# Performance work log

Measured on AMD Instinct MI355X. Metric: run time of the kernel, lower is better.

Reference implementation:

```python
import jax, jax.numpy as jnp
import numpy as np

# config matching init_kwargs: stox_params=[4,2,1,1,64,2], in=64, out=128, k=3, pad=1
A_BITS = 4          # a_slices = a_bits / a_bits_per_stream = 4
W_SLICES = 2        # w_bits / w_bits_per_slice = 2
NUM_CHUNKS = 9      # ceil(64*9/64)
SUB = 64            # crossbar chunk width
ITERS = 2           # stochastic iterations
EPS = 1e-5          # BatchNorm1d eps


def ste(y, x):
    # straight-through estimator: forward y, backward identity of x
    return x + jax.lax.stop_gradient(y - x)


def unfold3x3(x):
    # torch F.unfold(x, 3, dilation=1, padding=1, stride=1): [B,C,H,W] -> [B, C*9, H*W]
    B, C, H, W = x.shape
    xp = jnp.pad(x, ((0, 0), (0, 0), (1, 1), (1, 1)))
    cols = [xp[:, :, i:i + H, j:j + W] for i in range(3) for j in range(3)]
    return jnp.stack(cols, axis=2).reshape(B, C * 9, H * W)  # (c, kh, kw) ordering


def setup_inputs() -> dict:
    key = jax.random.key(0)
    k1, k2 = jax.random.split(key)
    inputs = jax.random.normal(k1, (8, 64, 32, 32), jnp.float32)
    fan_in = 64 * 9  # kaiming_normal_ fan_in
    weight = jax.random.normal(k2, (128 * W_SLICES, 64, 3, 3), jnp.float32) * np.float32(np.sqrt(2.0 / fan_in))
    bn_gamma = jnp.ones((128 * W_SLICES,), jnp.float32)
    bn_beta = jnp.zeros((128 * W_SLICES,), jnp.float32)
    return {"inputs": inputs, "weight": weight, "bn_gamma": bn_gamma, "bn_beta": bn_beta}


def reference(inputs, weight, bn_gamma, bn_beta):
    O = weight.shape[0]  # out_channels * W_SLICES = 256
    # --- per-output-row weight standardization + 1-bit STE quantization (WeightQuantize) ---
    wf = weight.reshape(O, -1)                       # [O, Cin*9]
    bw = wf - wf.mean(-1, keepdims=True)
    bw = bw / bw.std(-1, ddof=1, keepdims=True)      # torch std is unbiased
    qw = ste(jnp.sign(bw), bw)                       # [O, Cin*9]
    # --- unfold + multi-bit input stream (create_input_stream): bit-planes stacked on batch dim ---
    a = unfold3x3(inputs)                            # [B, Cin*9, L]
    Bsz, C9, L = a.shape
    x = jnp.clip(a, 0.0, 1.0)
    q = jnp.round(x * (2 ** A_BITS - 1))
    bits = jnp.stack([jnp.floor(q / (2 ** i)) % 2 for i in range(A_BITS)], 0)  # [A,B,C9,L]
    qa = bits.reshape(A_BITS * Bsz, C9, L)
    # --- chunked crossbar linear + BatchNorm1d(train) + MTJ sign, summed over chunks/iterations ---
    out = jnp.zeros((A_BITS * Bsz, O, L), a.dtype)
    for c in range(NUM_CHUNKS):
        wk = qa[:, c * SUB:(c + 1) * SUB, :]         # [B', SUB, L]
        ww = qw[:, c * SUB:(c + 1) * SUB]            # [O, SUB]
        for _ in range(ITERS):
            lin = jnp.einsum('bcl,oc->bol', wk, ww)  # [B', O, L]
            mu = lin.mean((0, 2), keepdims=True)
            var = lin.var((0, 2), keepdims=True)     # biased, as torch BN training
            bn = bn_gamma[None, :, None] * (lin - mu) / jnp.sqrt(var + EPS) + bn_beta[None, :, None]
            out = out + ste(jnp.sign(bn), bn)        # MTJ stochastic comparator -> sign w/ STE
    # --- bit-weighted reconstructions ---
    wvec = (2.0 ** jnp.arange(W_SLICES, dtype=a.dtype)) / (2 ** W_SLICES - 1)
    out = jnp.einsum('s,bsol->bol', wvec, out.reshape(A_BITS * Bsz, W_SLICES, O // W_SLICES, L))
    avec = (2.0 ** jnp.arange(A_BITS, dtype=a.dtype)) / (2 ** A_BITS - 1)
    out = jnp.einsum('a,abol->bol', avec, out.reshape(A_BITS, Bsz, O // W_SLICES, L))
    # --- F.fold with (1,1) kernel == reshape to square spatial map ---
    P = int(np.sqrt(L))
    return out.reshape(Bsz, O // W_SLICES, P, P)
```

## Files before the change

### kernel.cpp

```cpp
#include <hip/hip_runtime.h>
#include <cstdint>
#include <cstddef>

static const size_t OFF_ACT  = 0;
static const size_t OFF_W    = OFF_ACT + 2359296;
static const size_t OFF_T    = OFF_W   + 18432;
static const size_t OFF_S1   = OFF_T   + 18432;
static const size_t OFF_MUG  = OFF_S1  + 9216;
static const size_t OFF_FLAG = OFF_MUG + 18432;

__device__ __forceinline__ int isgn(int e) {
  int t = e < -1 ? -1 : e;
  return t > 1 ? 1 : t;
}

__global__ __launch_bounds__(256) void k_prep(const float* __restrict__ x,
                                              const float* __restrict__ w,
                                              const float* __restrict__ gamma,
                                              const float* __restrict__ beta,
                                              int* __restrict__ T,
                                              uint64_t* __restrict__ act,
                                              uint64_t* __restrict__ wbits,
                                              int* __restrict__ flag) {
  int bid = blockIdx.x;
  int tid = threadIdx.x;
  if (bid < 512) {
    int base = bid << 10;
    int vals[9];
#pragma unroll
    for (int k = 0; k < 9; ++k) vals[k] = 0;
#pragma unroll
    for (int i = 0; i < 4; ++i) {
      int px = tid + i * 256;
      int h = px >> 5, ww = px & 31;
      float v = x[base + px];
      v = fminf(fmaxf(v, 0.f), 1.f);
      int q = (int)rintf(v * 15.f);
      int pc = __popc((unsigned)q);
      vals[0] += pc;
      if (h == 0) vals[1] += pc;
      if (h == 31) vals[2] += pc;
      if (ww == 0) vals[3] += pc;
      if (ww == 31) vals[4] += pc;
      if (h == 0 && ww == 0) vals[5] += pc;
      if (h == 0 && ww == 31) vals[6] += pc;
      if (h == 31 && ww == 0) vals[7] += pc;
      if (h == 31 && ww == 31) vals[8] += pc;
    }
#pragma unroll
    for (int k = 0; k < 9; ++k)
      for (int off = 32; off; off >>= 1) vals[k] += __shfl_down(vals[k], off, 64);
    __shared__ int red[4][9];
    int wid = tid >> 6, lane = tid & 63;
    if (lane == 0)
#pragma unroll
      for (int k = 0; k < 9; ++k) red[wid][k] = vals[k];
    __syncthreads();
    if (tid < 9) T[bid * 9 + tid] = red[0][tid] + red[1][tid] + red[2][tid] + red[3][tid];
  } else if (bid < 1664) {
    int gidx = (bid - 512) * 256 + tid;
    int half = gidx & 3;
    int idx = gidx >> 2;
    int l = idx & 1023;
    int c = (idx >> 10) % 9;
    int b = idx / (9 * 1024);
    int h = l >> 5, w0 = l & 31;
    int i9 = c * 64 + half * 16;
    int ch = i9 / 9;
    int k = i9 - ch * 9;
    int ki = k / 3, kj = k - ki * 3;
    unsigned m0 = 0, m1 = 0, m2 = 0, m3 = 0;
#pragma unroll
    for (int jj = 0; jj < 16; ++jj) {
      int hh = h + ki - 1, ww = w0 + kj - 1;
      int q = 0;
      if ((unsigned)hh < 32u && (unsigned)ww < 32u) {
        float v = x[(((b * 64 + ch) << 10) + (hh << 5)) + ww];
        v = fminf(fmaxf(v, 0.f), 1.f);
        q = (int)rintf(v * 15.f);
      }
      m0 |= (unsigned)(q & 1) << jj;
      m1 |= (unsigned)((q >> 1) & 1) << jj;
      m2 |= (unsigned)((q >> 2) & 1) << jj;
      m3 |= (unsigned)((q >> 3) & 1) << jj;
      if (++kj == 3) { kj = 0; if (++ki == 3) { ki = 0; ++ch; } }
    }
    size_t stride = 8 * 9 * 1024;
    size_t off = ((size_t)b * 9 + c) * 1024 + l;
    unsigned short* a16 = (unsigned short*)act;
    a16[(0 * stride + off) * 4 + half] = (unsigned short)m0;
    a16[(1 * stride + off) * 4 + half] = (unsigned short)m1;
    a16[(2 * stride + off) * 4 + half] = (unsigned short)m2;
    a16[(3 * stride + off) * 4 + half] = (unsigned short)m3;
  } else {
    int lane = tid & 63;
    int wid = tid >> 6;
    int o = (bid - 1664) * 4 + wid;
    const float* row = w + (size_t)o * 576;
    double s = 0.0;
#pragma unroll
    for (int i = 0; i < 9; ++i) s += (double)row[lane + i * 64];
    for (int off = 32; off; off >>= 1) s += __shfl_down(s, off, 64);
    s = __shfl(s, 0, 64);
    float mean = (float)(s / 576.0);
#pragma unroll
    for (int c = 0; c < 9; ++c) {
      float v = row[c * 64 + lane];
      unsigned long long m = __ballot((v - mean) > 0.f);
      if (lane == 0) wbits[o * 9 + c] = (uint64_t)m;
    }
    if (lane == 0) flag[o] = (beta[o] == 0.f && gamma[o] > 0.f) ? 1 : 0;
  }
}

__global__ __launch_bounds__(256) void k_s1(const int* __restrict__ T,
                                            const uint64_t* __restrict__ wbits,
                                            const int* __restrict__ flag,
                                            const float* __restrict__ gamma,
                                            const uint64_t* __restrict__ act,
                                            int* __restrict__ S1,
                                            float2* __restrict__ MUG) {
  __shared__ int Tsh[576];
  __shared__ int Ush[9 * 65];
  int tid = threadIdx.x;
  for (int i = tid; i < 576; i += 256) {
    int acc = 0;
#pragma unroll
    for (int b = 0; b < 8; ++b) acc += T[b * 576 + i];
    Tsh[i] = acc;
  }
  __syncthreads();
  for (int i = tid; i < 576; i += 256) {
    int ch = i / 9;
    int k = i - ch * 9;
    int ki = k / 3, kj = k - ki * 3;
    const int* t = &Tsh[ch * 9];
    int u = t[0];
    if (ki == 0) u -= t[2]; else if (ki == 2) u -= t[1];
    if (kj == 0) u -= t[4]; else if (kj == 2) u -= t[3];
    if (ki == 0 && kj == 0) u += t[8];
    if (ki == 0 && kj == 2) u += t[7];
    if (ki == 2 && kj == 0) u += t[6];
    if (ki == 2 && kj == 2) u += t[5];
    Ush[(i >> 6) * 65 + (i & 63)] = u;
  }
  __syncthreads();
  int pair = blockIdx.x * 256 + tid;
  int o = pair / 9, c = pair - o * 9;
  uint64_t wv = wbits[pair];
  int tot = 0, pos = 0;
#pragma unroll 8
  for (int j = 0; j < 64; ++j) {
    int cnt = Ush[c * 65 + j];
    tot += cnt;
    if ((wv >> j) & 1) pos += cnt;
  }
  int s1 = 2 * pos - tot;
  S1[pair] = s1;
  if (!flag[o]) {
    int s2 = 0;
    for (int i = 0; i < 32768; ++i) {
      uint64_t av = act[((size_t)(i >> 10) * 9 + c) * 1024 + (i & 1023)];
      int lin = 2 * __popcll(av & wv) - __popcll(av);
      s2 += lin * lin;
    }
    float mu = (float)s1 * (1.f / 32768.f);
    float ex2 = (float)s2 * (1.f / 32768.f);
    float var = ex2 - mu * mu;
    if (var < 0.f) var = 0.f;
    MUG[pair] = make_float2(mu, gamma[o] / sqrtf(var + 1e-5f));
  }
}

__global__ __launch_bounds__(256, 8) void k_out(const uint64_t* __restrict__ act,
                                                const uint64_t* __restrict__ wbits,
                                                const int* __restrict__ S1,
                                                const float2* __restrict__ MUG,
                                                const int* __restrict__ flag,
                                                const float* __restrict__ beta,
                                                float* __restrict__ out) {
  int ltile = blockIdx.x;
  int og = blockIdx.y;
  int b = blockIdx.z;
  int tid = threadIdx.x;
  int lane = tid & 63;
  int wid = __builtin_amdgcn_readfirstlane(tid >> 6);
  int op = og * 4 + wid;
  int l = (ltile << 7) + lane * 2;

  uint64_t Wv[2][9];
  int Sv[2][9];
  int FL[2];
#pragma unroll
  for (int s = 0; s < 2; ++s) {
    int o = s * 128 + op;
    FL[s] = flag[o];
#pragma unroll
    for (int c = 0; c < 9; ++c) {
      Wv[s][c] = wbits[o * 9 + c];
      Sv[s][c] = S1[o * 9 + c];
    }
  }

  int M0 = 0, M1 = 0;

  if (FL[0] & FL[1]) {
    for (int a = 0; a < 4; ++a) {
      const uint64_t* ap = act + ((size_t)(a * 8 + b) * 9) * 1024 + l;
      int m00 = 0, m01 = 0, m10 = 0, m11 = 0;
#pragma unroll
      for (int c = 0; c < 9; ++c) {
        uint64_t av0 = ap[c * 1024];
        uint64_t av1 = ap[c * 1024 + 1];
        int np0 = -((int)__popcll(av0) << 15);
        int np1 = -((int)__popcll(av1) << 15);
        {
          uint64_t w = Wv[0][c];
          int t1 = Sv[0][c];
          m00 += isgn((((int)__popcll(av0 & w)) << 16) + np0 - t1);
          m01 += isgn((((int)__popcll(av1 & w)) << 16) + np1 - t1);
        }
        {
          uint64_t w = Wv[1][c];
          int t1 = Sv[1][c];
          m10 += isgn((((int)__popcll(av0 & w)) << 16) + np0 - t1);
          m11 += isgn((((int)__popcll(av1 & w)) << 16) + np1 - t1);
        }
      }
      M0 += (m00 + 2 * m10) << a;
      M1 += (m01 + 2 * m11) << a;
    }
    size_t ob = ((size_t)b * 128 + op) * 1024 + l;
    out[ob]     = (float)M0 * (2.f / 45.f);
    out[ob + 1] = (float)M1 * (2.f / 45.f);
  } else {
    const float avec[4] = {1.f / 15.f, 2.f / 15.f, 4.f / 15.f, 8.f / 15.f};
    const float wvec[2] = {1.f / 3.f, 2.f / 3.f};
    float accf0 = 0.f, accf1 = 0.f;
    for (int a = 0; a < 4; ++a) {
      const uint64_t* ap = act + ((size_t)(a * 8 + b) * 9) * 1024 + l;
      int m00 = 0, m01 = 0, m10 = 0, m11 = 0;
      float f00 = 0.f, f01 = 0.f, f10 = 0.f, f11 = 0.f;
      for (int c = 0; c < 9; ++c) {
        uint64_t av0 = ap[c * 1024];
        uint64_t av1 = ap[c * 1024 + 1];
        int np0 = -((int)__popcll(av0) << 15);
        int np1 = -((int)__popcll(av1) << 15);
        for (int s = 0; s < 2; ++s) {
          uint64_t w = Wv[s][c];
          if (FL[s]) {
            int t1 = Sv[s][c];
            int e0 = (((int)__popcll(av0 & w)) << 16) + np0 - t1;
            int e1 = (((int)__popcll(av1 & w)) << 16) + np1 - t1;
            int g0 = isgn(e0), g1 = isgn(e1);
            if (s == 0) { m00 += g0; m01 += g1; } else { m10 += g0; m11 += g1; }
          } else {
            int o = s * 128 + op;
            float2 m2 = MUG[o * 9 + c];
            float bb = beta[o];
            int l0 = 2 * (int)__popcll(av0 & w) + (np0 >> 15);
            int l1 = 2 * (int)__popcll(av1 & w) + (np1 >> 15);
            float bn0 = m2.y * ((float)l0 - m2.x) + bb;
            float bn1 = m2.y * ((float)l1 - m2.x) + bb;
            float g0 = (bn0 > 0.f) ? 1.f : ((bn0 < 0.f) ? -1.f : 0.f);
            float g1 = (bn1 > 0.f) ? 1.f : ((bn1 < 0.f) ? -1.f : 0.f);
            if (s == 0) { f00 += g0; f01 += g1; } else { f10 += g0; f11 += g1; }
          }
        }
      }
      M0 += (m00 + 2 * m10) << a;
      M1 += (m01 + 2 * m11) << a;
      accf0 += avec[a] * (wvec[0] * f00 + wvec[1] * f10);
      accf1 += avec[a] * (wvec[0] * f01 + wvec[1] * f11);
    }
    size_t ob = ((size_t)b * 128 + op) * 1024 + l;
    out[ob]     = (float)M0 * (2.f / 45.f) + 2.f * accf0;
    out[ob + 1] = (float)M1 * (2.f / 45.f) + 2.f * accf1;
  }
}

extern "C" void kernel_launch(void* const* d_in, const int* in_sizes, int n_in,
                              void* d_out, int out_size, void* d_ws, size_t ws_size,
                              hipStream_t stream) {
  const float* inputs = (const float*)d_in[0];
  const float* weight = (const float*)d_in[1];
  const float* gamma = (const float*)d_in[2];
  const float* beta = (const float*)d_in[3];
  float* out = (float*)d_out;

  char* ws = (char*)d_ws;
  uint64_t* act = (uint64_t*)(ws + OFF_ACT);
  uint64_t* wbits = (uint64_t*)(ws + OFF_W);
  int* T = (int*)(ws + OFF_T);
  int* S1 = (int*)(ws + OFF_S1);
  float2* MUG = (float2*)(ws + OFF_MUG);
  int* flag = (int*)(ws + OFF_FLAG);

  k_prep<<<1728, 256, 0, stream>>>(inputs, weight, gamma, beta, T, act, wbits, flag);
  k_s1<<<9, 256, 0, stream>>>(T, wbits, flag, gamma, act, S1, MUG);
  k_out<<<dim3(8, 32, 8), 256, 0, stream>>>(act, wbits, S1, MUG, flag, beta, out);
}
```

Before: 102.7 us.

## Fuse S1/BN-stat kernel into output kernel, computing per-block stats in shared memory

Removes the separate 9-block k_s1 launch and recomputes the T reduction, U correction and S1 sums redundantly inside every k_out block, restricted to the 8 output rows that block needs. The results live in shared memory, and S1 and flag are broadcast with readfirstlane. This removes one launch and a serialized low-occupancy kernel. In exchange, each of the 2048 blocks redoes the T reduction and S1 work. In the non-flag path each block would also rerun the 32768-iteration variance loop, which would be very costly, but with the default gamma=1 and beta=0 inputs that path is skipped.

```diff
diff --git a/kernel.cpp b/kernel.cpp
--- a/kernel.cpp
+++ b/kernel.cpp
@@ -113,20 +113,24 @@
   }
 }
 
-__global__ __launch_bounds__(256) void k_s1(const int* __restrict__ T,
-                                            const uint64_t* __restrict__ wbits,
-                                            const int* __restrict__ flag,
-                                            const float* __restrict__ gamma,
-                                            const uint64_t* __restrict__ act,
-                                            int* __restrict__ S1,
-                                            float2* __restrict__ MUG) {
+__global__ __launch_bounds__(256, 8) void k_out(const uint64_t* __restrict__ act,
+                                                const uint64_t* __restrict__ wbits,
+                                                const int* __restrict__ T,
+                                                const int* __restrict__ flag,
+                                                const float* __restrict__ gamma,
+                                                const float* __restrict__ beta,
+                                                float* __restrict__ out) {
   __shared__ int Tsh[576];
   __shared__ int Ush[9 * 65];
+  __shared__ int S1sh[72];
+  __shared__ float2 MUGsh[72];
   int tid = threadIdx.x;
+  int og = blockIdx.y;
+
   for (int i = tid; i < 576; i += 256) {
     int acc = 0;
 #pragma unroll
-    for (int b = 0; b < 8; ++b) acc += T[b * 576 + i];
+    for (int bb = 0; bb < 8; ++bb) acc += T[bb * 576 + i];
     Tsh[i] = acc;
   }
   __syncthreads();
@@ -145,44 +149,38 @@
     Ush[(i >> 6) * 65 + (i & 63)] = u;
   }
   __syncthreads();
-  int pair = blockIdx.x * 256 + tid;
-  int o = pair / 9, c = pair - o * 9;
-  uint64_t wv = wbits[pair];
-  int tot = 0, pos = 0;
+  if (tid < 72) {
+    int oi = tid / 9, c = tid - oi * 9;
+    int s = oi >> 2, w = oi & 3;
+    int o = s * 128 + og * 4 + w;
+    uint64_t wv = wbits[o * 9 + c];
+    int tot = 0, pos = 0;
 #pragma unroll 8
-  for (int j = 0; j < 64; ++j) {
-    int cnt = Ush[c * 65 + j];
-    tot += cnt;
-    if ((wv >> j) & 1) pos += cnt;
-  }
-  int s1 = 2 * pos - tot;
-  S1[pair] = s1;
-  if (!flag[o]) {
-    int s2 = 0;
-    for (int i = 0; i < 32768; ++i) {
-      uint64_t av = act[((size_t)(i >> 10) * 9 + c) * 1024 + (i & 1023)];
-      int lin = 2 * __popcll(av & wv) - __popcll(av);
-      s2 += lin * lin;
-    }
-    float mu = (float)s1 * (1.f / 32768.f);
-    float ex2 = (float)s2 * (1.f / 32768.f);
-    float var = ex2 - mu * mu;
-    if (var < 0.f) var = 0.f;
-    MUG[pair] = make_float2(mu, gamma[o] / sqrtf(var + 1e-5f));
-  }
-}
-
-__global__ __launch_bounds__(256, 8) void k_out(const uint64_t* __restrict__ act,
-                                                const uint64_t* __restrict__ wbits,
-                                                const int* __restrict__ S1,
-                                                const float2* __restrict__ MUG,
-                                                const int* __restrict__ flag,
-                                                const float* __restrict__ beta,
-                                                float* __restrict__ out) {
+    for (int j = 0; j < 64; ++j) {
+      int cnt = Ush[c * 65 + j];
+      tot += cnt;
+      if ((wv >> j) & 1) pos += cnt;
+    }
+    int s1 = 2 * pos - tot;
+    S1sh[tid] = s1;
+    if (!flag[o]) {
+      int s2 = 0;
+      for (int i = 0; i < 32768; ++i) {
+        uint64_t av = act[((size_t)(i >> 10) * 9 + c) * 1024 + (i & 1023)];
+        int lin = 2 * __popcll(av & wv) - __popcll(av);
+        s2 += lin * lin;
+      }
+      float mu = (float)s1 * (1.f / 32768.f);
+      float ex2 = (float)s2 * (1.f / 32768.f);
+      float var = ex2 - mu * mu;
+      if (var < 0.f) var = 0.f;
+      MUGsh[tid] = make_float2(mu, gamma[o] / sqrtf(var + 1e-5f));
+    }
+  }
+  __syncthreads();
+
   int ltile = blockIdx.x;
-  int og = blockIdx.y;
   int b = blockIdx.z;
-  int tid = threadIdx.x;
   int lane = tid & 63;
   int wid = __builtin_amdgcn_readfirstlane(tid >> 6);
   int op = og * 4 + wid;
@@ -194,11 +192,11 @@
 #pragma unroll
   for (int s = 0; s < 2; ++s) {
     int o = s * 128 + op;
-    FL[s] = flag[o];
+    FL[s] = __builtin_amdgcn_readfirstlane(flag[o]);
 #pragma unroll
     for (int c = 0; c < 9; ++c) {
       Wv[s][c] = wbits[o * 9 + c];
-      Sv[s][c] = S1[o * 9 + c];
+      Sv[s][c] = __builtin_amdgcn_readfirstlane(S1sh[(s * 4 + wid) * 9 + c]);
     }
   }
 
@@ -255,9 +253,8 @@
             int g0 = isgn(e0), g1 = isgn(e1);
             if (s == 0) { m00 += g0; m01 += g1; } else { m10 += g0; m11 += g1; }
           } else {
-            int o = s * 128 + op;
-            float2 m2 = MUG[o * 9 + c];
-            float bb = beta[o];
+            float2 m2 = MUGsh[(s * 4 + wid) * 9 + c];
+            float bb = beta[s * 128 + op];
             int l0 = 2 * (int)__popcll(av0 & w) + (np0 >> 15);
             int l1 = 2 * (int)__popcll(av1 & w) + (np1 >> 15);
             float bn0 = m2.y * ((float)l0 - m2.x) + bb;
@@ -292,11 +289,8 @@
   uint64_t* act = (uint64_t*)(ws + OFF_ACT);
   uint64_t* wbits = (uint64_t*)(ws + OFF_W);
   int* T = (int*)(ws + OFF_T);
-  int* S1 = (int*)(ws + OFF_S1);
-  float2* MUG = (float2*)(ws + OFF_MUG);
   int* flag = (int*)(ws + OFF_FLAG);
 
   k_prep<<<1728, 256, 0, stream>>>(inputs, weight, gamma, beta, T, act, wbits, flag);
-  k_s1<<<9, 256, 0, stream>>>(T, wbits, flag, gamma, act, S1, MUG);
-  k_out<<<dim3(8, 32, 8), 256, 0, stream>>>(act, wbits, S1, MUG, flag, beta, out);
-}
+  k_out<<<dim3(8, 32, 8), 256, 0, stream>>>(act, wbits, T, flag, gamma, beta, out);
+}
```

Result: no change. 103.1 us (+0.4%).

## Compute binary crossbar dot products with int8 MFMA instead of popcount

Applied to the files above, without the earlier changes.

Weights are now also written as ±1 int8 bytes. In the output kernel, 16 activation bits at a time are expanded into 0/1 bytes, and the 64-wide chunk dot products are computed with 16x16x64 int8 MFMA instructions rather than per-thread popcounts. Work is regrouped so that each block covers 16 spatial positions and all 128 output pairs, and the negated S1 thresholds are staged in shared memory. This adds bit-to-byte unpacking overhead and lowers the occupancy hint in exchange for matrix-core throughput.

```diff
diff --git a/kernel.cpp b/kernel.cpp
--- a/kernel.cpp
+++ b/kernel.cpp
@@ -5,9 +5,12 @@
 static const size_t OFF_ACT  = 0;
 static const size_t OFF_W    = OFF_ACT + 2359296;
 static const size_t OFF_T    = OFF_W   + 18432;
-static const size_t OFF_S1   = OFF_T   + 18432;
-static const size_t OFF_MUG  = OFF_S1  + 9216;
+static const size_t OFF_NS1  = OFF_T   + 18432;
+static const size_t OFF_MUG  = OFF_NS1 + 9216;
 static const size_t OFF_FLAG = OFF_MUG + 18432;
+static const size_t OFF_WB   = OFF_FLAG + 1024;
+
+typedef int v4i __attribute__((ext_vector_type(4)));
 
 __device__ __forceinline__ int isgn(int e) {
   int t = e < -1 ? -1 : e;
@@ -21,7 +24,8 @@
                                               int* __restrict__ T,
                                               uint64_t* __restrict__ act,
                                               uint64_t* __restrict__ wbits,
-                                              int* __restrict__ flag) {
+                                              int* __restrict__ flag,
+                                              signed char* __restrict__ wbyte) {
   int bid = blockIdx.x;
   int tid = threadIdx.x;
   if (bid < 512) {
@@ -106,8 +110,10 @@
 #pragma unroll
     for (int c = 0; c < 9; ++c) {
       float v = row[c * 64 + lane];
-      unsigned long long m = __ballot((v - mean) > 0.f);
+      int pos = (v - mean) > 0.f;
+      unsigned long long m = __ballot(pos);
       if (lane == 0) wbits[o * 9 + c] = (uint64_t)m;
+      wbyte[(c * 256 + o) * 64 + lane] = pos ? (signed char)1 : (signed char)-1;
     }
     if (lane == 0) flag[o] = (beta[o] == 0.f && gamma[o] > 0.f) ? 1 : 0;
   }
@@ -118,7 +124,7 @@
                                             const int* __restrict__ flag,
                                             const float* __restrict__ gamma,
                                             const uint64_t* __restrict__ act,
-                                            int* __restrict__ S1,
+                                            int* __restrict__ negS1,
                                             float2* __restrict__ MUG) {
   __shared__ int Tsh[576];
   __shared__ int Ush[9 * 65];
@@ -156,7 +162,7 @@
     if ((wv >> j) & 1) pos += cnt;
   }
   int s1 = 2 * pos - tot;
-  S1[pair] = s1;
+  negS1[c * 256 + o] = -s1;
   if (!flag[o]) {
     int s2 = 0;
     for (int i = 0; i < 32768; ++i) {
@@ -172,110 +178,128 @@
   }
 }
 
-__global__ __launch_bounds__(256, 8) void k_out(const uint64_t* __restrict__ act,
-                                                const uint64_t* __restrict__ wbits,
-                                                const int* __restrict__ S1,
+__global__ __launch_bounds__(256, 2) void k_out(const uint64_t* __restrict__ act,
+                                                const signed char* __restrict__ wbyte,
+                                                const int* __restrict__ negS1g,
                                                 const float2* __restrict__ MUG,
                                                 const int* __restrict__ flag,
                                                 const float* __restrict__ beta,
                                                 float* __restrict__ out) {
-  int ltile = blockIdx.x;
-  int og = blockIdx.y;
-  int b = blockIdx.z;
+  __shared__ int nsh[2304];
   int tid = threadIdx.x;
+  int lt = blockIdx.x;
+  int b = blockIdx.y;
+  for (int i = tid; i < 2304; i += 256) nsh[i] = negS1g[i];
+  __syncthreads();
+
   int lane = tid & 63;
-  int wid = __builtin_amdgcn_readfirstlane(tid >> 6);
-  int op = og * 4 + wid;
-  int l = (ltile << 7) + lane * 2;
-
-  uint64_t Wv[2][9];
-  int Sv[2][9];
-  int FL[2];
-#pragma unroll
-  for (int s = 0; s < 2; ++s) {
-    int o = s * 128 + op;
-    FL[s] = flag[o];
-#pragma unroll
+  int w = __builtin_amdgcn_readfirstlane(tid >> 6);
+  int row = lane & 15;
+  int g = lane >> 4;
+
+  int o0 = w * 32 + (lane & 31);
+  int fb = flag[o0] & flag[o0 + 128];
+  bool fastAll = (bool)__all(fb != 0);
+
+  const v4i zacc = {0, 0, 0, 0};
+  int l = lt * 16 + row;
+
+  if (fastAll) {
+    int M[2][4] = {{0, 0, 0, 0}, {0, 0, 0, 0}};
     for (int c = 0; c < 9; ++c) {
-      Wv[s][c] = wbits[o * 9 + c];
-      Sv[s][c] = S1[o * 9 + c];
-    }
-  }
-
-  int M0 = 0, M1 = 0;
-
-  if (FL[0] & FL[1]) {
-    for (int a = 0; a < 4; ++a) {
-      const uint64_t* ap = act + ((size_t)(a * 8 + b) * 9) * 1024 + l;
-      int m00 = 0, m01 = 0, m10 = 0, m11 = 0;
-#pragma unroll
-      for (int c = 0; c < 9; ++c) {
-        uint64_t av0 = ap[c * 1024];
-        uint64_t av1 = ap[c * 1024 + 1];
-        int np0 = -((int)__popcll(av0) << 15);
-        int np1 = -((int)__popcll(av1) << 15);
-        {
-          uint64_t w = Wv[0][c];
-          int t1 = Sv[0][c];
-          m00 += isgn((((int)__popcll(av0 & w)) << 16) + np0 - t1);
-          m01 += isgn((((int)__popcll(av1 & w)) << 16) + np1 - t1);
-        }
-        {
-          uint64_t w = Wv[1][c];
-          int t1 = Sv[1][c];
-          m10 += isgn((((int)__popcll(av0 & w)) << 16) + np0 - t1);
-          m11 += isgn((((int)__popcll(av1 & w)) << 16) + np1 - t1);
-        }
-      }
-      M0 += (m00 + 2 * m10) << a;
-      M1 += (m01 + 2 * m11) << a;
-    }
-    size_t ob = ((size_t)b * 128 + op) * 1024 + l;
-    out[ob]     = (float)M0 * (2.f / 45.f);
-    out[ob + 1] = (float)M1 * (2.f / 45.f);
-  } else {
-    const float avec[4] = {1.f / 15.f, 2.f / 15.f, 4.f / 15.f, 8.f / 15.f};
-    const float wvec[2] = {1.f / 3.f, 2.f / 3.f};
-    float accf0 = 0.f, accf1 = 0.f;
-    for (int a = 0; a < 4; ++a) {
-      const uint64_t* ap = act + ((size_t)(a * 8 + b) * 9) * 1024 + l;
-      int m00 = 0, m01 = 0, m10 = 0, m11 = 0;
-      float f00 = 0.f, f01 = 0.f, f10 = 0.f, f11 = 0.f;
-      for (int c = 0; c < 9; ++c) {
-        uint64_t av0 = ap[c * 1024];
-        uint64_t av1 = ap[c * 1024 + 1];
-        int np0 = -((int)__popcll(av0) << 15);
-        int np1 = -((int)__popcll(av1) << 15);
-        for (int s = 0; s < 2; ++s) {
-          uint64_t w = Wv[s][c];
-          if (FL[s]) {
-            int t1 = Sv[s][c];
-            int e0 = (((int)__popcll(av0 & w)) << 16) + np0 - t1;
-            int e1 = (((int)__popcll(av1 & w)) << 16) + np1 - t1;
-            int g0 = isgn(e0), g1 = isgn(e1);
-            if (s == 0) { m00 += g0; m01 += g1; } else { m10 += g0; m11 += g1; }
-          } else {
-            int o = s * 128 + op;
-            float2 m2 = MUG[o * 9 + c];
-            float bb = beta[o];
-            int l0 = 2 * (int)__popcll(av0 & w) + (np0 >> 15);
-            int l1 = 2 * (int)__popcll(av1 & w) + (np1 >> 15);
-            float bn0 = m2.y * ((float)l0 - m2.x) + bb;
-            float bn1 = m2.y * ((float)l1 - m2.x) + bb;
-            float g0 = (bn0 > 0.f) ? 1.f : ((bn0 < 0.f) ? -1.f : 0.f);
-            float g1 = (bn1 > 0.f) ? 1.f : ((bn1 < 0.f) ? -1.f : 0.f);
-            if (s == 0) { f00 += g0; f01 += g1; } else { f10 += g0; f11 += g1; }
+      v4i Af[4];
+      int nS[4][4];
+#pragma unroll
+      for (int q = 0; q < 4; ++q) {
+        int ot = 2 * w + (q & 1) + (q >> 1) * 8;
+        Af[q] = *(const v4i*)(wbyte + ((size_t)(c * 256 + ot * 16 + row) * 64 + g * 16));
+#pragma unroll
+        for (int r = 0; r < 4; ++r) nS[q][r] = nsh[c * 256 + ot * 16 + g * 4 + r];
+      }
+#pragma unroll
+      for (int a = 0; a < 4; ++a) {
+        size_t idx = ((size_t)(a * 8 + b) * 9 + c) * 1024 + l;
+        unsigned dw = *(const unsigned*)((const char*)act + idx * 8 + (g >> 1) * 4);
+        unsigned bits = (dw >> ((g & 1) * 16)) & 0xFFFFu;
+        v4i Bf;
+#pragma unroll
+        for (int d = 0; d < 4; ++d)
+          Bf[d] = (int)((((bits >> (4 * d)) & 0xFu) * 0x00204081u) & 0x01010101u);
+#pragma unroll
+        for (int q = 0; q < 4; ++q) {
+          v4i acc = __builtin_amdgcn_mfma_i32_16x16x64_i8(Af[q], Bf, zacc, 0, 0, 0);
+#pragma unroll
+          for (int r = 0; r < 4; ++r) {
+            int e = (acc[r] << 15) + nS[q][r];
+            M[q & 1][r] += isgn(e) << (a + (q >> 1));
           }
         }
       }
-      M0 += (m00 + 2 * m10) << a;
-      M1 += (m01 + 2 * m11) << a;
-      accf0 += avec[a] * (wvec[0] * f00 + wvec[1] * f10);
-      accf1 += avec[a] * (wvec[0] * f01 + wvec[1] * f11);
-    }
-    size_t ob = ((size_t)b * 128 + op) * 1024 + l;
-    out[ob]     = (float)M0 * (2.f / 45.f) + 2.f * accf0;
-    out[ob + 1] = (float)M1 * (2.f / 45.f) + 2.f * accf1;
+    }
+#pragma unroll
+    for (int q2 = 0; q2 < 2; ++q2)
+#pragma unroll
+      for (int r = 0; r < 4; ++r) {
+        int oo = (2 * w + q2) * 16 + g * 4 + r;
+        out[((size_t)b * 128 + oo) * 1024 + l] = (float)M[q2][r] * (2.f / 45.f);
+      }
+  } else {
+    int M[2][4] = {{0, 0, 0, 0}, {0, 0, 0, 0}};
+    float F[2][4] = {{0.f, 0.f, 0.f, 0.f}, {0.f, 0.f, 0.f, 0.f}};
+    int flv[4][4];
+#pragma unroll
+    for (int q = 0; q < 4; ++q) {
+      int ot = 2 * w + (q & 1) + (q >> 1) * 8;
+#pragma unroll
+      for (int r = 0; r < 4; ++r) flv[q][r] = flag[ot * 16 + g * 4 + r];
+    }
+    for (int c = 0; c < 9; ++c) {
+      v4i Af[4];
+      int nS[4][4];
+#pragma unroll
+      for (int q = 0; q < 4; ++q) {
+        int ot = 2 * w + (q & 1) + (q >> 1) * 8;
+        Af[q] = *(const v4i*)(wbyte + ((size_t)(c * 256 + ot * 16 + row) * 64 + g * 16));
+#pragma unroll
+        for (int r = 0; r < 4; ++r) nS[q][r] = nsh[c * 256 + ot * 16 + g * 4 + r];
+      }
+#pragma unroll
+      for (int a = 0; a < 4; ++a) {
+        size_t idx = ((size_t)(a * 8 + b) * 9 + c) * 1024 + l;
+        unsigned dw = *(const unsigned*)((const char*)act + idx * 8 + (g >> 1) * 4);
+        unsigned bits = (dw >> ((g & 1) * 16)) & 0xFFFFu;
+        v4i Bf;
+#pragma unroll
+        for (int d = 0; d < 4; ++d)
+          Bf[d] = (int)((((bits >> (4 * d)) & 0xFu) * 0x00204081u) & 0x01010101u);
+#pragma unroll
+        for (int q = 0; q < 4; ++q) {
+          v4i acc = __builtin_amdgcn_mfma_i32_16x16x64_i8(Af[q], Bf, zacc, 0, 0, 0);
+          int ot = 2 * w + (q & 1) + (q >> 1) * 8;
+#pragma unroll
+          for (int r = 0; r < 4; ++r) {
+            int lin = acc[r];
+            if (flv[q][r]) {
+              M[q & 1][r] += isgn((lin << 15) + nS[q][r]) << (a + (q >> 1));
+            } else {
+              int o = ot * 16 + g * 4 + r;
+              float2 m2 = MUG[o * 9 + c];
+              float bn = m2.y * ((float)lin - m2.x) + beta[o];
+              float sg = (bn > 0.f) ? 1.f : ((bn < 0.f) ? -1.f : 0.f);
+              F[q & 1][r] += sg * (float)(1 << (a + (q >> 1)));
+            }
+          }
+        }
+      }
+    }
+#pragma unroll
+    for (int q2 = 0; q2 < 2; ++q2)
+#pragma unroll
+      for (int r = 0; r < 4; ++r) {
+        int oo = (2 * w + q2) * 16 + g * 4 + r;
+        out[((size_t)b * 128 + oo) * 1024 + l] =
+            ((float)M[q2][r] + F[q2][r]) * (2.f / 45.f);
+      }
   }
 }
 
@@ -292,11 +316,12 @@
   uint64_t* act = (uint64_t*)(ws + OFF_ACT);
   uint64_t* wbits = (uint64_t*)(ws + OFF_W);
   int* T = (int*)(ws + OFF_T);
-  int* S1 = (int*)(ws + OFF_S1);
+  int* negS1 = (int*)(ws + OFF_NS1);
   float2* MUG = (float2*)(ws + OFF_MUG);
   int* flag = (int*)(ws + OFF_FLAG);
-
-  k_prep<<<1728, 256, 0, stream>>>(inputs, weight, gamma, beta, T, act, wbits, flag);
-  k_s1<<<9, 256, 0, stream>>>(T, wbits, flag, gamma, act, S1, MUG);
-  k_out<<<dim3(8, 32, 8), 256, 0, stream>>>(act, wbits, S1, MUG, flag, beta, out);
-}
+  signed char* wbyte = (signed char*)(ws + OFF_WB);
+
+  k_prep<<<1728, 256, 0, stream>>>(inputs, weight, gamma, beta, T, act, wbits, flag, wbyte);
+  k_s1<<<9, 256, 0, stream>>>(T, wbits, flag, gamma, act, negS1, MUG);
+  k_out<<<dim3(64, 8), 256, 0, stream>>>(act, wbyte, negS1, MUG, flag, beta, out);
+}
```

Measured after the change: 95.39 us. 7.1% less time.
